# Kernel tuning notes

Hardware: AMD Instinct MI355X
Metric: run time of the kernel (lower is better)

## Reference

```python
import jax, jax.numpy as jnp
import numpy as np
from functools import partial

K_SPARSE = 50  # k_sparse passed as int to __init__
EPS = 1e-12    # numerical guard inside sqrt (diagonal zeros)


def setup_inputs() -> dict:
    key = jax.random.key(0)
    k1, k2, k3, k4 = jax.random.split(key, 4)
    B, n, D = 16, 1000, 128
    locs = jax.random.uniform(k1, (B, n, 2), dtype=jnp.float32)
    init_embeddings = jax.random.normal(k2, (B, n, D), dtype=jnp.float32)
    W = jax.random.normal(k3, (1, D), dtype=jnp.float32) * 0.1  # nn.Linear(1, D).weight.T
    b = jax.random.normal(k4, (D,), dtype=jnp.float32) * 0.1    # nn.Linear bias
    return {"locs": locs, "init_embeddings": init_embeddings, "W": W, "b": b}


def _sparsify(dist):
    """Per-node top-k nearest neighbors (no self loops).
    dist: [B, n, n] -> (neighbor_idx [B, n, k], edge_attr [B, n, k])."""
    B, n, _ = dist.shape
    # mask self loops with +inf so they are never selected
    diag = jnp.eye(n, dtype=bool)
    masked = jnp.where(diag[None, :, :], jnp.inf, dist)
    neg_vals, idx = jax.lax.top_k(-masked, K_SPARSE)  # k smallest distances
    return idx, -neg_vals


def reference(locs, init_embeddings, W, b):
    B, n, _ = locs.shape
    D = init_embeddings.shape[-1]
    k = K_SPARSE

    # pairwise Euclidean distance matrix [B, n, n]
    diff = locs[:, :, None, :] - locs[:, None, :, :]
    dist = jnp.sqrt(jnp.sum(diff * diff, axis=-1) + EPS)

    nbr_idx, edge_attr = _sparsify(dist)  # [B, n, k] each

    # PyG Batch: concatenate graphs with node-index offsets of index * n
    offsets = (jnp.arange(B, dtype=jnp.int32) * n)[:, None]            # [B, 1]
    src = jnp.broadcast_to(jnp.arange(n, dtype=jnp.int32)[:, None], (n, k))
    src = (src.reshape(1, n * k) + offsets).reshape(-1)                # [B*n*k]
    dst = (nbr_idx.reshape(B, n * k).astype(jnp.int32) + offsets).reshape(-1)
    edge_index = jnp.stack([src, dst], axis=0)                          # [2, B*n*k]

    # edge_embed: Linear(1, D) on scalar distances
    edge_emb = edge_attr.reshape(-1, 1) @ W + b                         # [B*n*k, D]

    x = init_embeddings.reshape(B * n, D)                               # batched node feats
    return x, edge_index, edge_emb
```

## Files before the change

kernel.cpp:

```cpp
#include <hip/hip_runtime.h>
#include <cstdint>
#include <cstddef>


namespace {

constexpr int kB  = 16;
constexpr int kN  = 1000;
constexpr int kD  = 128;
constexpr int kK  = 50;
constexpr int kCPL = 16;
constexpr int kNodesPerBlock = 4;
constexpr int kBlocksPerBatch = kN / kNodesPerBlock;

__global__ __launch_bounds__(256)
void tsp_edge_kernel(const float* __restrict__ locs,
                     const float* __restrict__ init_emb,
                     const float* __restrict__ W,
                     const float* __restrict__ bias,
                     float* __restrict__ out)
{
#pragma clang fp contract(off)
  const int tid  = threadIdx.x;
  const int wave = tid >> 6;
  const int lane = tid & 63;
  const int blk  = blockIdx.x;
  const int b    = blk / kBlocksPerBatch;
  const int node_in_b = (blk % kBlocksPerBatch) * kNodesPerBlock + wave;
  const int node = b * kN + node_in_b;

  __shared__ float2 sloc[kN];
  const float2* gl = reinterpret_cast<const float2*>(locs) + (size_t)b * kN;
  for (int t = tid; t < kN; t += 256) sloc[t] = gl[t];
  __syncthreads();

  const float2 my = sloc[node_in_b];

  float d[kCPL];
  const int jbase = lane * kCPL;
#pragma unroll
  for (int s = 0; s < kCPL; ++s) {
    const int j = jbase + s;
    const bool valid = (j < kN) && (j != node_in_b);
    const float2 pj = sloc[(j < kN) ? j : 0];
    const float dx = my.x - pj.x;
    const float dy = my.y - pj.y;
    const float d2 = dx * dx + dy * dy;
    const float dd = sqrtf(d2 + 1e-12f);
    d[s] = valid ? dd : INFINITY;
  }

  float best = d[0];
  int bslot = 0;
#pragma unroll
  for (int s = 1; s < kCPL; ++s) {
    if (d[s] < best) { best = d[s]; bslot = s; }
  }

  float res_d = 0.0f;
  int   res_j = 0;
#pragma unroll 1
  for (int r = 0; r < kK; ++r) {
    float m = best;
#pragma unroll
    for (int off = 32; off >= 1; off >>= 1) m = fminf(m, __shfl_xor(m, off, 64));
    const unsigned long long msk = __ballot(best == m);
    const int owner = __ffsll(msk) - 1;
    const int oslot = __shfl(bslot, owner, 64);
    const int jwin  = owner * kCPL + oslot;
    if (lane == r) { res_d = m; res_j = jwin; }
    if (lane == owner) {
#pragma unroll
      for (int s = 0; s < kCPL; ++s) { if (s == oslot) d[s] = INFINITY; }
      best = d[0]; bslot = 0;
#pragma unroll
      for (int s = 1; s < kCPL; ++s) {
        if (d[s] < best) { best = d[s]; bslot = s; }
      }
    }
  }

  constexpr size_t X_SZ    = (size_t)kB * kN * kD;
  constexpr size_t E_SZ    = (size_t)kB * kN * kK;
  constexpr size_t SRC_OFF = X_SZ;
  constexpr size_t DST_OFF = X_SZ + E_SZ;
  constexpr size_t EMB_OFF = X_SZ + 2 * E_SZ;

  {
    const float2* srcp = reinterpret_cast<const float2*>(init_emb + (size_t)node * kD);
    float2* dstp = reinterpret_cast<float2*>(out + (size_t)node * kD);
    dstp[lane] = srcp[lane];
  }

  if (lane < kK) {
    out[SRC_OFF + (size_t)node * kK + lane] = (float)node;
    out[DST_OFF + (size_t)node * kK + lane] = (float)(b * kN + res_j);
  }

  const int colg = (lane & 31) * 4;
  const float4 wv = *reinterpret_cast<const float4*>(W + colg);
  const float4 bv = *reinterpret_cast<const float4*>(bias + colg);
  float* ebase = out + EMB_OFF + (size_t)node * (kK * kD);
#pragma unroll
  for (int rr = 0; rr < kK / 2; ++rr) {
    const int r0 = 2 * rr + (lane >> 5);
    const float a = __shfl(res_d, r0, 64);
    float4 v;
    v.x = a * wv.x + bv.x;
    v.y = a * wv.y + bv.y;
    v.z = a * wv.z + bv.z;
    v.w = a * wv.w + bv.w;
    *reinterpret_cast<float4*>(ebase + (size_t)r0 * kD + colg) = v;
  }
}

}

extern "C" void kernel_launch(void* const* d_in, const int* in_sizes, int n_in,
                              void* d_out, int out_size, void* d_ws, size_t ws_size,
                              hipStream_t stream) {
  const float* locs = (const float*)d_in[0];
  const float* emb  = (const float*)d_in[1];
  const float* W    = (const float*)d_in[2];
  const float* bias = (const float*)d_in[3];
  float* out = (float*)d_out;

  dim3 grid(kB * kBlocksPerBatch);
  dim3 block(256);
  hipLaunchKernelGGL(tsp_edge_kernel, grid, block, 0, stream, locs, emb, W, bias, out);
}
```

Measured before the change: 502.4 us.

## Pack distance and index into 64-bit keys and presort per-lane candidates

Packs each distance and column index into one double-typed 64-bit key so a single fmin wave reduction yields both the winner and its index, with no ballot or owner shuffle. Each lane bitonic-sorts its 16 keys up front, so after a win the owner just shifts its array instead of rescanning for the new minimum. Candidates are strided across lanes, and each round writes its embedding row immediately as float2 stores, which removes the trailing shuffle loop. The cost is 64-bit shuffles and double fmin/fmax, which are slower than fp32 on some hardware, plus extra register pressure from the 16 doubles.

```diff
diff --git a/kernel.cpp b/kernel.cpp
--- a/kernel.cpp
+++ b/kernel.cpp
@@ -12,6 +12,12 @@
 constexpr int kCPL = 16;
 constexpr int kNodesPerBlock = 4;
 constexpr int kBlocksPerBatch = kN / kNodesPerBlock;
+
+__device__ __forceinline__ double pack_key(float dd, int j) {
+  const unsigned long long u =
+      ((unsigned long long)__float_as_uint(dd) << 32) | (unsigned)j;
+  return __longlong_as_double((long long)u);
+}
 
 __global__ __launch_bounds__(256)
 void tsp_edge_kernel(const float* __restrict__ locs,
@@ -30,52 +36,44 @@
   const int node = b * kN + node_in_b;
 
   __shared__ float2 sloc[kN];
-  const float2* gl = reinterpret_cast<const float2*>(locs) + (size_t)b * kN;
-  for (int t = tid; t < kN; t += 256) sloc[t] = gl[t];
+  {
+    const float4* gl4 = reinterpret_cast<const float4*>(locs + (size_t)b * kN * 2);
+    float4* sl4 = reinterpret_cast<float4*>(sloc);
+    for (int t = tid; t < kN / 2; t += 256) sl4[t] = gl4[t];
+  }
   __syncthreads();
 
   const float2 my = sloc[node_in_b];
 
-  float d[kCPL];
-  const int jbase = lane * kCPL;
+  double key[kCPL];
 #pragma unroll
   for (int s = 0; s < kCPL; ++s) {
-    const int j = jbase + s;
+    const int j = lane + (s << 6);
     const bool valid = (j < kN) && (j != node_in_b);
     const float2 pj = sloc[(j < kN) ? j : 0];
     const float dx = my.x - pj.x;
     const float dy = my.y - pj.y;
     const float d2 = dx * dx + dy * dy;
-    const float dd = sqrtf(d2 + 1e-12f);
-    d[s] = valid ? dd : INFINITY;
+    float dd = sqrtf(d2 + 1e-12f);
+    if (!valid) dd = INFINITY;
+    key[s] = pack_key(dd, j);
   }
 
-  float best = d[0];
-  int bslot = 0;
 #pragma unroll
-  for (int s = 1; s < kCPL; ++s) {
-    if (d[s] < best) { best = d[s]; bslot = s; }
-  }
-
-  float res_d = 0.0f;
-  int   res_j = 0;
-#pragma unroll 1
-  for (int r = 0; r < kK; ++r) {
-    float m = best;
+  for (int kk = 2; kk <= kCPL; kk <<= 1) {
 #pragma unroll
-    for (int off = 32; off >= 1; off >>= 1) m = fminf(m, __shfl_xor(m, off, 64));
-    const unsigned long long msk = __ballot(best == m);
-    const int owner = __ffsll(msk) - 1;
-    const int oslot = __shfl(bslot, owner, 64);
-    const int jwin  = owner * kCPL + oslot;
-    if (lane == r) { res_d = m; res_j = jwin; }
-    if (lane == owner) {
+    for (int jj = kk >> 1; jj > 0; jj >>= 1) {
 #pragma unroll
-      for (int s = 0; s < kCPL; ++s) { if (s == oslot) d[s] = INFINITY; }
-      best = d[0]; bslot = 0;
-#pragma unroll
-      for (int s = 1; s < kCPL; ++s) {
-        if (d[s] < best) { best = d[s]; bslot = s; }
+      for (int i = 0; i < kCPL; ++i) {
+        const int l2 = i ^ jj;
+        if (l2 > i) {
+          const double a  = key[i];
+          const double c  = key[l2];
+          const double lo = fmin(a, c);
+          const double hi = fmax(a, c);
+          if ((i & kk) == 0) { key[i] = lo; key[l2] = hi; }
+          else               { key[i] = hi; key[l2] = lo; }
+        }
       }
     }
   }
@@ -86,6 +84,37 @@
   constexpr size_t DST_OFF = X_SZ + E_SZ;
   constexpr size_t EMB_OFF = X_SZ + 2 * E_SZ;
 
+  const float2 wv = reinterpret_cast<const float2*>(W)[lane];
+  const float2 bv = reinterpret_cast<const float2*>(bias)[lane];
+  float* ebase = out + EMB_OFF + (size_t)node * (kK * kD);
+  const int col2 = lane * 2;
+
+  int res_j = 0;
+  const double INFK = __builtin_inf();
+
+#pragma unroll 1
+  for (int r = 0; r < kK; ++r) {
+    double m = key[0];
+#pragma unroll
+    for (int off = 32; off >= 1; off >>= 1)
+      m = fmin(m, __shfl_xor(m, off, 64));
+
+    const unsigned long long u = (unsigned long long)__double_as_longlong(m);
+    const float dist = __uint_as_float((unsigned)(u >> 32));
+    if (lane == r) res_j = (int)(u & 0xFFFFFFFFull);
+
+    float2 v;
+    v.x = dist * wv.x + bv.x;
+    v.y = dist * wv.y + bv.y;
+    *reinterpret_cast<float2*>(ebase + (size_t)r * kD + col2) = v;
+
+    if (key[0] == m) {
+#pragma unroll
+      for (int s = 0; s < kCPL - 1; ++s) key[s] = key[s + 1];
+      key[kCPL - 1] = INFK;
+    }
+  }
+
   {
     const float2* srcp = reinterpret_cast<const float2*>(init_emb + (size_t)node * kD);
     float2* dstp = reinterpret_cast<float2*>(out + (size_t)node * kD);
@@ -95,22 +124,6 @@
   if (lane < kK) {
     out[SRC_OFF + (size_t)node * kK + lane] = (float)node;
     out[DST_OFF + (size_t)node * kK + lane] = (float)(b * kN + res_j);
-  }
-
-  const int colg = (lane & 31) * 4;
-  const float4 wv = *reinterpret_cast<const float4*>(W + colg);
-  const float4 bv = *reinterpret_cast<const float4*>(bias + colg);
-  float* ebase = out + EMB_OFF + (size_t)node * (kK * kD);
-#pragma unroll
-  for (int rr = 0; rr < kK / 2; ++rr) {
-    const int r0 = 2 * rr + (lane >> 5);
-    const float a = __shfl(res_d, r0, 64);
-    float4 v;
-    v.x = a * wv.x + bv.x;
-    v.y = a * wv.y + bv.y;
-    v.z = a * wv.z + bv.z;
-    v.w = a * wv.w + bv.w;
-    *reinterpret_cast<float4*>(ebase + (size_t)r0 * kD + colg) = v;
   }
 }
 
```

Result: faster. 468.9 us (-6.7%).
